# Performance work log

Hardware: AMD Instinct MI355X
Metric: run time of the kernel (lower is better)

## Reference

```python
import jax, jax.numpy as jnp
import numpy as np

SIZE = 128
N = 262144


def _softplus(x):
    # matches torch: log(1 + exp(x)) with B = 1
    return jnp.log1p(jnp.exp(x))


def setup_inputs() -> dict:
    key = jax.random.key(0)
    k1, k2 = jax.random.split(key)
    inputs = jax.random.normal(k1, (N, 2 * SIZE), dtype=jnp.float32)
    targets = jax.random.normal(k2, (N, SIZE), dtype=jnp.float32)
    max_logvar = jnp.ones((1, SIZE), dtype=jnp.float32)       # init +1
    min_logvar = -jnp.ones((1, SIZE), dtype=jnp.float32)      # init -1
    return {"inputs": inputs, "targets": targets,
            "max_logvar": max_logvar, "min_logvar": min_logvar}


def reference(inputs, targets, max_logvar, min_logvar):
    mean = inputs[:, :SIZE]                    # [N, SIZE]
    logvar = inputs[:, SIZE:]                  # [N, SIZE]
    # soft-clamp logvar into [min_logvar, max_logvar]
    logvar = max_logvar - _softplus(max_logvar - logvar)
    logvar = min_logvar + _softplus(logvar - min_logvar)
    var = jnp.exp(logvar)
    diff = mean - targets
    mid = diff / var
    lg = jnp.sum(logvar)
    # trace(diff @ mid.T) == sum(diff * mid): same math, O(N*D) not O(N^2*D)
    out = jnp.sum(diff * mid) + lg
    return out
```

## Files before the change

kernel.cpp:

```cpp
#include <hip/hip_runtime.h>
#include <hip/hip_bf16.h>

#define SIZE 128
#define NBLOCKS 8192

__global__ __launch_bounds__(256) void probloss_partial(
    const float4* __restrict__ inputs,
    const float4* __restrict__ targets,
    const float4* __restrict__ maxlv,
    const float4* __restrict__ minlv,
    float* __restrict__ part,
    int nrows)
{
    const int gtid    = blockIdx.x * blockDim.x + threadIdx.x;
    const int cg      = gtid & 31;
    const int row0    = gtid >> 5;
    const int rstride = (gridDim.x * blockDim.x) >> 5;

    float4 a = maxlv[cg];
    float4 b = minlv[cg];
    float ena[4], eb[4];
    #pragma unroll
    for (int k = 0; k < 4; ++k) {
        ena[k] = __expf(-(&a.x)[k]);
        eb[k]  = __expf((&b.x)[k]);
    }

    float acc = 0.0f;
    for (int r = row0; r < nrows; r += rstride) {
        float4 m  = inputs[r * 64 + cg];
        float4 lv = inputs[r * 64 + 32 + cg];
        float4 tg = targets[r * 32 + cg];

        float prod = 1.0f;
        #pragma unroll
        for (int k = 0; k < 4; ++k) {
            float d   = (&m.x)[k] - (&tg.x)[k];
            float t   = __expf(-(&lv.x)[k]);
            float s   = ena[k] + t;
            float u   = __builtin_fmaf(eb[k], s, 1.0f);
            float inv = s * __builtin_amdgcn_rcpf(u);
            acc  += d * d * inv;
            prod *= inv;
        }
        acc -= __logf(prod);
    }

    #pragma unroll
    for (int off = 32; off > 0; off >>= 1)
        acc += __shfl_down(acc, off);

    __shared__ float smem[4];
    const int lane = threadIdx.x & 63;
    const int wid  = threadIdx.x >> 6;
    if (lane == 0) smem[wid] = acc;
    __syncthreads();
    if (threadIdx.x == 0)
        part[blockIdx.x] = smem[0] + smem[1] + smem[2] + smem[3];
}

__global__ __launch_bounds__(256) void probloss_final(
    const float4* __restrict__ part, float* __restrict__ out)
{
    float acc = 0.0f;
    for (int i = threadIdx.x; i < NBLOCKS / 4; i += 256) {
        float4 v = part[i];
        acc += (v.x + v.y) + (v.z + v.w);
    }
    #pragma unroll
    for (int off = 32; off > 0; off >>= 1)
        acc += __shfl_down(acc, off);

    __shared__ float smem[4];
    const int lane = threadIdx.x & 63;
    const int wid  = threadIdx.x >> 6;
    if (lane == 0) smem[wid] = acc;
    __syncthreads();
    if (threadIdx.x == 0)
        out[0] = smem[0] + smem[1] + smem[2] + smem[3];
}

extern "C" void kernel_launch(void* const* d_in, const int* in_sizes, int n_in,
                              void* d_out, int out_size, void* d_ws, size_t ws_size,
                              hipStream_t stream) {
    const float4* inputs  = (const float4*)d_in[0];
    const float4* targets = (const float4*)d_in[1];
    const float4* maxlv   = (const float4*)d_in[2];
    const float4* minlv   = (const float4*)d_in[3];
    float* out  = (float*)d_out;
    float* part = (float*)d_ws;

    const int nrows = in_sizes[1] / SIZE;

    probloss_partial<<<NBLOCKS, 256, 0, stream>>>(inputs, targets, maxlv, minlv,
                                                  part, nrows);
    probloss_final<<<1, 256, 0, stream>>>((const float4*)part, out);
}
```

Baseline: 75.51 us.

## Fuse final reduction into main kernel via last-block atomic counter

Replaces the separate single-block final reduction kernel with a last-block-done pattern: each block writes its partial sum, fences, and bumps an atomic counter, and the last block to finish reduces all partials. The grid is halved so each thread handles more rows and there are fewer partials to reduce. This removes one kernel launch and its boundary, but adds a memset launch to reset the counter plus an atomic and fences per block.

After: 281.2 us. 272% more time.

```diff
diff --git a/kernel.cpp b/kernel.cpp
--- a/kernel.cpp
+++ b/kernel.cpp
@@ -2,14 +2,34 @@
 #include <hip/hip_bf16.h>
 
 #define SIZE 128
-#define NBLOCKS 8192
+#define NBLOCKS 4096
 
-__global__ __launch_bounds__(256) void probloss_partial(
+__device__ __forceinline__ void body4(float4 m, float4 lv, float4 tg,
+                                      const float* __restrict__ ena,
+                                      const float* __restrict__ eb,
+                                      float& acc) {
+    float prod = 1.0f;
+    #pragma unroll
+    for (int k = 0; k < 4; ++k) {
+        float d   = (&m.x)[k] - (&tg.x)[k];
+        float t   = __expf(-(&lv.x)[k]);
+        float s   = ena[k] + t;
+        float u   = __builtin_fmaf(eb[k], s, 1.0f);
+        float inv = s * __builtin_amdgcn_rcpf(u);
+        acc  += d * d * inv;
+        prod *= inv;
+    }
+    acc -= __logf(prod);
+}
+
+__global__ __launch_bounds__(256) void probloss_fused(
     const float4* __restrict__ inputs,
     const float4* __restrict__ targets,
     const float4* __restrict__ maxlv,
     const float4* __restrict__ minlv,
     float* __restrict__ part,
+    unsigned* __restrict__ counter,
+    float* __restrict__ out,
     int nrows)
 {
     const int gtid    = blockIdx.x * blockDim.x + threadIdx.x;
@@ -28,22 +48,8 @@
 
     float acc = 0.0f;
     for (int r = row0; r < nrows; r += rstride) {
-        float4 m  = inputs[r * 64 + cg];
-        float4 lv = inputs[r * 64 + 32 + cg];
-        float4 tg = targets[r * 32 + cg];
-
-        float prod = 1.0f;
-        #pragma unroll
-        for (int k = 0; k < 4; ++k) {
-            float d   = (&m.x)[k] - (&tg.x)[k];
-            float t   = __expf(-(&lv.x)[k]);
-            float s   = ena[k] + t;
-            float u   = __builtin_fmaf(eb[k], s, 1.0f);
-            float inv = s * __builtin_amdgcn_rcpf(u);
-            acc  += d * d * inv;
-            prod *= inv;
-        }
-        acc -= __logf(prod);
+        body4(inputs[r * 64 + cg], inputs[r * 64 + 32 + cg],
+              targets[r * 32 + cg], ena, eb, acc);
     }
 
     #pragma unroll
@@ -51,33 +57,32 @@
         acc += __shfl_down(acc, off);
 
     __shared__ float smem[4];
+    __shared__ bool amLast;
     const int lane = threadIdx.x & 63;
     const int wid  = threadIdx.x >> 6;
     if (lane == 0) smem[wid] = acc;
     __syncthreads();
-    if (threadIdx.x == 0)
+    if (threadIdx.x == 0) {
         part[blockIdx.x] = smem[0] + smem[1] + smem[2] + smem[3];
-}
+        __threadfence();
+        unsigned prev = atomicAdd(counter, 1u);
+        amLast = (prev == (unsigned)(gridDim.x - 1));
+    }
+    __syncthreads();
 
-__global__ __launch_bounds__(256) void probloss_final(
-    const float4* __restrict__ part, float* __restrict__ out)
-{
-    float acc = 0.0f;
-    for (int i = threadIdx.x; i < NBLOCKS / 4; i += 256) {
-        float4 v = part[i];
-        acc += (v.x + v.y) + (v.z + v.w);
+    if (amLast) {
+        __threadfence();
+        float facc = 0.0f;
+        for (int i = threadIdx.x; i < NBLOCKS; i += 256)
+            facc += part[i];
+        #pragma unroll
+        for (int off = 32; off > 0; off >>= 1)
+            facc += __shfl_down(facc, off);
+        if (lane == 0) smem[wid] = facc;
+        __syncthreads();
+        if (threadIdx.x == 0)
+            out[0] = smem[0] + smem[1] + smem[2] + smem[3];
     }
-    #pragma unroll
-    for (int off = 32; off > 0; off >>= 1)
-        acc += __shfl_down(acc, off);
-
-    __shared__ float smem[4];
-    const int lane = threadIdx.x & 63;
-    const int wid  = threadIdx.x >> 6;
-    if (lane == 0) smem[wid] = acc;
-    __syncthreads();
-    if (threadIdx.x == 0)
-        out[0] = smem[0] + smem[1] + smem[2] + smem[3];
 }
 
 extern "C" void kernel_launch(void* const* d_in, const int* in_sizes, int n_in,
@@ -87,12 +92,13 @@
     const float4* targets = (const float4*)d_in[1];
     const float4* maxlv   = (const float4*)d_in[2];
     const float4* minlv   = (const float4*)d_in[3];
-    float* out  = (float*)d_out;
-    float* part = (float*)d_ws;
+    float* out      = (float*)d_out;
+    float* part     = (float*)d_ws;
+    unsigned* counter = (unsigned*)((char*)d_ws + NBLOCKS * sizeof(float));
 
     const int nrows = in_sizes[1] / SIZE;
 
-    probloss_partial<<<NBLOCKS, 256, 0, stream>>>(inputs, targets, maxlv, minlv,
-                                                  part, nrows);
-    probloss_final<<<1, 256, 0, stream>>>((const float4*)part, out);
+    hipMemsetAsync(counter, 0, sizeof(unsigned), stream);
+    probloss_fused<<<NBLOCKS, 256, 0, stream>>>(inputs, targets, maxlv, minlv,
+                                                part, counter, out, nrows);
 }
```
